# Kernel tuning notes

Measured on AMD Instinct MI355X. Metric: run time of the kernel, lower is better.

## Reference

```python
import jax, jax.numpy as jnp
import numpy as np

RNN = 128
IN = 2
OUT = 2
OBS_LEN = 8
PRED_LEN = 12


def setup_inputs() -> dict:
    key = jax.random.key(0)
    ks = jax.random.split(key, 8)
    B = 32768
    s = 1.0 / np.sqrt(RNN)  # pytorch LSTM/Linear init bound
    u = lambda k, shape: jax.random.uniform(k, shape, jnp.float32, -s, s)
    return {
        "traj_in": jax.random.normal(ks[0], (B, OBS_LEN, IN), jnp.float32),
        "traj_gt": jax.random.normal(ks[1], (B, PRED_LEN, OUT), jnp.float32),
        "W_ih": u(ks[2], (4 * RNN, IN)),
        "W_hh": u(ks[3], (4 * RNN, RNN)),
        "b_ih": u(ks[4], (4 * RNN,)),
        "b_hh": u(ks[5], (4 * RNN,)),
        "W_last": u(ks[6], (OUT, RNN)),
        "b_last": u(ks[7], (OUT,)),
    }


def _lstm_cell(x, h, c, W_ih, W_hh, b_ih, b_hh):
    # PyTorch gate order: i, f, g, o
    gates = x @ W_ih.T + h @ W_hh.T + (b_ih + b_hh)  # [B, 4*RNN]
    i, f, g, o = jnp.split(gates, 4, axis=-1)
    i = jax.nn.sigmoid(i)
    f = jax.nn.sigmoid(f)
    g = jnp.tanh(g)
    o = jax.nn.sigmoid(o)
    c2 = f * c + i * g
    h2 = o * jnp.tanh(c2)
    return h2, c2


def reference(traj_in, traj_gt, W_ih, W_hh, b_ih, b_hh, W_last, b_last):
    B = traj_in.shape[0]
    dt = traj_in.dtype
    h0 = jnp.zeros((B, RNN), dt)
    c0 = jnp.zeros((B, RNN), dt)

    def head(h):
        # relu -> dropout (identity in eval) -> linear
        return jax.nn.relu(h) @ W_last.T + b_last

    def obs_step(carry, x_t):
        h, c = carry
        h, c = _lstm_cell(x_t, h, c, W_ih, W_hh, b_ih, b_hh)
        return (h, c), head(h)

    xs = jnp.swapaxes(traj_in, 0, 1)  # [T, B, 2]
    (h, c), obs_preds = jax.lax.scan(obs_step, (h0, c0), xs)
    traj_t = obs_preds[-1]  # prediction from last observed step

    def pred_step(carry, _):
        t, h, c = carry
        h2, c2 = _lstm_cell(t, h, c, W_ih, W_hh, b_ih, b_hh)
        return (head(h2), h2, c2), t  # emit current pred, then advance

    _, ys = jax.lax.scan(pred_step, (traj_t, h, c), None, length=PRED_LEN)
    traj_pred = jnp.swapaxes(ys, 0, 1)  # [B, pred_len, 2]
    loss = jnp.mean((traj_pred - traj_gt) ** 2)
    return traj_pred, loss
```

## Files before the change

kernel.cpp:

```cpp
#include <hip/hip_runtime.h>

#define OBS 8
#define PREDL 12
#define NCELL 19

#define W_OFF     0
#define H_OFF     98304
#define RH_OFF    131072
#define LDS_BYTES 163840

typedef short short8 __attribute__((ext_vector_type(8)));
typedef float f32x16 __attribute__((ext_vector_type(16)));
struct U128 { unsigned a, b, c, d; };

__device__ __forceinline__ float sigm(float x) {
    return __builtin_amdgcn_rcpf(1.0f + __builtin_amdgcn_exp2f(x * -1.4426950408889634f));
}
__device__ __forceinline__ float tanh_(float x) {
    return __builtin_amdgcn_rcpf(1.0f + __builtin_amdgcn_exp2f(x * -2.8853900817779268f)) * 2.0f - 1.0f;
}
__device__ __forceinline__ unsigned f2bf(float f) {
    unsigned u = __builtin_bit_cast(unsigned, f);
    u += 0x7fffu + ((u >> 16) & 1u);
    return u >> 16;
}
__device__ __forceinline__ unsigned cvtpk(float lo, float hi) {
    unsigned r;
    asm("v_cvt_pk_bf16_f32 %0, %1, %2" : "=v"(r) : "v"(lo), "v"(hi));
    return r;
}

__global__ __attribute__((amdgpu_waves_per_eu(2, 2))) __launch_bounds__(512)
void lstm_persist(const float* __restrict__ traj_in, const float* __restrict__ traj_gt,
                  const float* __restrict__ W_ih, const float* __restrict__ W_hh,
                  const float* __restrict__ b_ih, const float* __restrict__ b_hh,
                  const float* __restrict__ W_last, const float* __restrict__ b_last,
                  float* __restrict__ out, float* __restrict__ wsloss)
{
    extern __shared__ char smem[];
    const int tid  = threadIdx.x;
    const int lane = tid & 63;
    const int wave = tid >> 6;
    const int l31  = lane & 31;
    const int half = lane >> 5;
    const int sw   = (l31 & 15) << 4;
    const int wm   = wave >> 2;
    const int wc   = wave & 3;
    const int col0 = wc * 32;
    const int myrow = wm * 32 + l31;

    for (int it = 0; it < 24; ++it) {
        int i = it * 512 + tid;
        int n = i >> 5, c4 = i & 31;
        const float4 w = *(const float4*)(W_hh + (size_t)n * 128 + c4 * 4);
        uint2 pk = { f2bf(w.x) | (f2bf(w.y) << 16), f2bf(w.z) | (f2bf(w.w) << 16) };
        *(uint2*)(smem + W_OFF + n * 256 + ((c4 * 8) ^ ((n & 15) << 4))) = pk;
    }

    short8 Ee[4];
    #pragma unroll
    for (int gg = 0; gg < 4; ++gg) {
        U128 v = { 0u, 0u, 0u, 0u };
        if (half == 0) {
            int n = gg * 128 + col0 + l31;
            float2 wi = *(const float2*)(W_ih + n * 2);
            float bsum = b_ih[n] + b_hh[n];
            v.a = f2bf(wi.x) | (f2bf(wi.y) << 16);
            v.b = f2bf(bsum);
        }
        Ee[gg] = __builtin_bit_cast(short8, v);
    }
    short8 Bo[8];
    #pragma unroll
    for (int ks = 0; ks < 8; ++ks) {
        const float* p = W_hh + (size_t)(384 + col0 + l31) * 128 + ks * 16 + half * 8;
        float4 u = *(const float4*)p;
        float4 v = *(const float4*)(p + 4);
        U128 q = { f2bf(u.x) | (f2bf(u.y) << 16), f2bf(u.z) | (f2bf(u.w) << 16),
                   f2bf(v.x) | (f2bf(v.y) << 16), f2bf(v.z) | (f2bf(v.w) << 16) };
        Bo[ks] = __builtin_bit_cast(short8, q);
    }
    short8 Wl[8];
    #pragma unroll
    for (int ks = 0; ks < 8; ++ks) {
        U128 q = { 0u, 0u, 0u, 0u };
        if (l31 < 2) {
            const float* p = W_last + l31 * 128 + ks * 16 + half * 8;
            float4 u = *(const float4*)p;
            float4 v = *(const float4*)(p + 4);
            q.a = f2bf(u.x) | (f2bf(u.y) << 16); q.b = f2bf(u.z) | (f2bf(u.w) << 16);
            q.c = f2bf(v.x) | (f2bf(v.y) << 16); q.d = f2bf(v.z) | (f2bf(v.w) << 16);
        }
        Wl[ks] = __builtin_bit_cast(short8, q);
    }
    const float bl0 = b_last[0], bl1 = b_last[1];

    f32x16 zacc{};
    float lossAcc = 0.f;

    for (int g = 0; g < 2; ++g) {
        const int rbase = blockIdx.x * 128 + g * 64;

        for (int i = 0; i < 8; ++i)
            *(unsigned*)(smem + H_OFF + (tid + i * 512) * 4) = 0u;
        __syncthreads();

        float c_[16];
        #pragma unroll
        for (int r = 0; r < 16; ++r) c_[r] = 0.f;

        for (int t = 0; t < NCELL; ++t) {
            const int hcur  = H_OFF  + (t & 1) * 16384;
            const int hnxt  = H_OFF  + ((t & 1) ^ 1) * 16384;
            const int rhcur = RH_OFF + (t & 1) * 16384;
            const int rhnxt = RH_OFF + ((t & 1) ^ 1) * 16384;

            float2 xx = make_float2(0.f, 0.f);
            if (t < OBS) {
                if (half == 0)
                    xx = *(const float2*)(traj_in + ((size_t)(rbase + myrow) * OBS + t) * 2);
            } else {
                short8 rb0 = *(const short8*)(smem + rhcur + myrow * 256 + ((half * 16) ^ sw));
                f32x16 hd = __builtin_amdgcn_mfma_f32_32x32x16_bf16(Wl[0], rb0, zacc, 0, 0, 0);
                #pragma unroll
                for (int ks = 1; ks < 8; ++ks) {
                    short8 rb = *(const short8*)(smem + rhcur + myrow * 256 +
                                                 ((ks * 32 + half * 16) ^ sw));
                    hd = __builtin_amdgcn_mfma_f32_32x32x16_bf16(Wl[ks], rb, hd, 0, 0, 0);
                }
                if (half == 0) {
                    xx.x = hd[0] + bl0;
                    xx.y = hd[1] + bl1;
                    if (wc == 0) {
                        size_t og = ((size_t)(rbase + myrow) * PREDL + (t - OBS)) * 2;
                        float2 gt = *(const float2*)(traj_gt + og);
                        *(float2*)(out + og) = xx;
                        float d0 = xx.x - gt.x, d1 = xx.y - gt.y;
                        lossAcc = fmaf(d0, d0, fmaf(d1, d1, lossAcc));
                    }
                }
            }

            short8 a[8];
            #pragma unroll
            for (int ks = 0; ks < 8; ++ks)
                a[ks] = *(const short8*)(smem + hcur + myrow * 256 + ((ks * 32 + half * 16) ^ sw));

            f32x16 ac0, ac1, ac2, ac3;
            {
                const int bb = (half * 16) ^ sw;
                const char* wb = smem + W_OFF + (col0 + l31) * 256 + bb;
                ac0 = __builtin_amdgcn_mfma_f32_32x32x16_bf16(a[0], *(const short8*)(wb),             zacc, 0, 0, 0);
                ac1 = __builtin_amdgcn_mfma_f32_32x32x16_bf16(a[0], *(const short8*)(wb + 128 * 256), zacc, 0, 0, 0);
                ac2 = __builtin_amdgcn_mfma_f32_32x32x16_bf16(a[0], *(const short8*)(wb + 256 * 256), zacc, 0, 0, 0);
                ac3 = __builtin_amdgcn_mfma_f32_32x32x16_bf16(a[0], Bo[0],                            zacc, 0, 0, 0);
            }
            #pragma unroll
            for (int ks = 1; ks < 8; ++ks) {
                const int bb = (ks * 32 + half * 16) ^ sw;
                const char* wb = smem + W_OFF + (col0 + l31) * 256 + bb;
                short8 bi  = *(const short8*)(wb);
                short8 bf_ = *(const short8*)(wb + 128 * 256);
                short8 bg  = *(const short8*)(wb + 256 * 256);
                ac0 = __builtin_amdgcn_mfma_f32_32x32x16_bf16(a[ks], bi,     ac0, 0, 0, 0);
                ac1 = __builtin_amdgcn_mfma_f32_32x32x16_bf16(a[ks], bf_,    ac1, 0, 0, 0);
                ac2 = __builtin_amdgcn_mfma_f32_32x32x16_bf16(a[ks], bg,     ac2, 0, 0, 0);
                ac3 = __builtin_amdgcn_mfma_f32_32x32x16_bf16(a[ks], Bo[ks], ac3, 0, 0, 0);
            }
            {
                unsigned xv = (half == 0) ? cvtpk(xx.x, xx.y) : 0u;
                U128 ax = { xv, (half == 0) ? 0x00003F80u : 0u, 0u, 0u };
                short8 aext = __builtin_bit_cast(short8, ax);
                ac0 = __builtin_amdgcn_mfma_f32_32x32x16_bf16(aext, Ee[0], ac0, 0, 0, 0);
                ac1 = __builtin_amdgcn_mfma_f32_32x32x16_bf16(aext, Ee[1], ac1, 0, 0, 0);
                ac2 = __builtin_amdgcn_mfma_f32_32x32x16_bf16(aext, Ee[2], ac2, 0, 0, 0);
                ac3 = __builtin_amdgcn_mfma_f32_32x32x16_bf16(aext, Ee[3], ac3, 0, 0, 0);
            }

            const bool doRelu = (t >= OBS - 1);
            #pragma unroll
            for (int r = 0; r < 16; ++r) {
                float iv = sigm(ac0[r]);
                float fv = sigm(ac1[r]);
                float gv = tanh_(ac2[r]);
                float ov = sigm(ac3[r]);
                float cv = fmaf(fv, c_[r], iv * gv);
                c_[r] = cv;
                float hv = ov * tanh_(cv);
                const int row  = (r & 3) + 8 * (r >> 2) + 4 * half;
                const int arow = wm * 32 + row;
                const int baddr = ((col0 + l31) * 2) ^ ((row & 15) << 4);
                float rl = fmaxf(hv, 0.f);
                unsigned hp = cvtpk(hv, rl);
                *(short*)(smem + hnxt + arow * 256 + baddr) = (short)hp;
                if (doRelu)
                    *(short*)(smem + rhnxt + arow * 256 + baddr) = (short)(hp >> 16);
            }
            __syncthreads();
        }

        if (wc == 0) {
            short8 rb0 = *(const short8*)(smem + RH_OFF + 16384 + myrow * 256 + ((half * 16) ^ sw));
            f32x16 hd = __builtin_amdgcn_mfma_f32_32x32x16_bf16(Wl[0], rb0, zacc, 0, 0, 0);
            #pragma unroll
            for (int ks = 1; ks < 8; ++ks) {
                short8 rb = *(const short8*)(smem + RH_OFF + 16384 + myrow * 256 +
                                             ((ks * 32 + half * 16) ^ sw));
                hd = __builtin_amdgcn_mfma_f32_32x32x16_bf16(Wl[ks], rb, hd, 0, 0, 0);
            }
            if (half == 0) {
                float o0 = hd[0] + bl0, o1 = hd[1] + bl1;
                size_t og = ((size_t)(rbase + myrow) * PREDL + (PREDL - 1)) * 2;
                float2 gt = *(const float2*)(traj_gt + og);
                *(float2*)(out + og) = make_float2(o0, o1);
                float d0 = o0 - gt.x, d1 = o1 - gt.y;
                lossAcc = fmaf(d0, d0, fmaf(d1, d1, lossAcc));
            }
        }
        __syncthreads();
    }

    #pragma unroll
    for (int s = 1; s < 64; s <<= 1) lossAcc += __shfl_xor(lossAcc, s, 64);
    float* sred = (float*)(smem + RH_OFF);
    if (lane == 0) sred[wave] = lossAcc;
    __syncthreads();
    if (tid == 0) {
        float s = 0.f;
        #pragma unroll
        for (int i = 0; i < 8; ++i) s += sred[i];
        wsloss[blockIdx.x] = s;
    }
}

__global__ void loss_reduce(const float* __restrict__ wsloss, float* __restrict__ out,
                            int npart, int nelem)
{
    __shared__ float sacc[4];
    int tid = threadIdx.x;
    float v = 0.f;
    for (int j = tid; j < npart; j += 256) v += wsloss[j];
    #pragma unroll
    for (int s = 1; s < 64; s <<= 1) v += __shfl_xor(v, s, 64);
    if ((tid & 63) == 0) sacc[tid >> 6] = v;
    __syncthreads();
    if (tid == 0) out[nelem] = (sacc[0] + sacc[1] + sacc[2] + sacc[3]) / (float)nelem;
}

extern "C" void kernel_launch(void* const* d_in, const int* in_sizes, int n_in,
                              void* d_out, int out_size, void* d_ws, size_t ws_size,
                              hipStream_t stream)
{
    const float* traj_in = (const float*)d_in[0];
    const float* traj_gt = (const float*)d_in[1];
    const float* W_ih    = (const float*)d_in[2];
    const float* W_hh    = (const float*)d_in[3];
    const float* b_ih    = (const float*)d_in[4];
    const float* b_hh    = (const float*)d_in[5];
    const float* W_last  = (const float*)d_in[6];
    const float* b_last  = (const float*)d_in[7];
    float* out = (float*)d_out;
    float* wsloss = (float*)d_ws;

    const int B      = in_sizes[0] / (OBS * 2);
    const int blocks = B / 128;

    lstm_persist<<<blocks, 512, LDS_BYTES, stream>>>(traj_in, traj_gt, W_ih, W_hh,
                                                     b_ih, b_hh, W_last, b_last,
                                                     out, wsloss);
    loss_reduce<<<1, 256, 0, stream>>>(wsloss, out, blocks, out_size - 1);
}
```

Measured before the change: 154.0 us.

## Fold activation scales into weights, interleave gate rows, precompute LDS addresses

Pre-multiplies the gate weights and biases by -log2(e), or -2·log2(e) for the g gate, so the sigmoid and tanh activations skip a multiply per element. It also interleaves the i/f/g weight rows in LDS so each column's three gates sit 256 bytes apart, and hoists all LDS addresses into precomputed per-thread arrays. The intent is to cut VALU work in the elementwise gate loop and address arithmetic in the inner loop. Rounding the pre-scaled weights to bf16 slightly changes numerics, and the address arrays add register pressure.

```diff
diff --git a/kernel.cpp b/kernel.cpp
--- a/kernel.cpp
+++ b/kernel.cpp
@@ -13,11 +13,11 @@
 typedef float f32x16 __attribute__((ext_vector_type(16)));
 struct U128 { unsigned a, b, c, d; };
 
-__device__ __forceinline__ float sigm(float x) {
-    return __builtin_amdgcn_rcpf(1.0f + __builtin_amdgcn_exp2f(x * -1.4426950408889634f));
-}
-__device__ __forceinline__ float tanh_(float x) {
-    return __builtin_amdgcn_rcpf(1.0f + __builtin_amdgcn_exp2f(x * -2.8853900817779268f)) * 2.0f - 1.0f;
+#define NL2E  (-1.4426950408889634f)
+#define N2L2E (-2.8853900817779268f)
+
+__device__ __forceinline__ float sigm_p(float y) {
+    return __builtin_amdgcn_rcpf(1.0f + __builtin_amdgcn_exp2f(y));
 }
 __device__ __forceinline__ unsigned f2bf(float f) {
     unsigned u = __builtin_bit_cast(unsigned, f);
@@ -52,9 +52,12 @@
     for (int it = 0; it < 24; ++it) {
         int i = it * 512 + tid;
         int n = i >> 5, c4 = i & 31;
+        int gi = n >> 7, cn = n & 127;
+        float sc = (gi == 2) ? N2L2E : NL2E;
         const float4 w = *(const float4*)(W_hh + (size_t)n * 128 + c4 * 4);
-        uint2 pk = { f2bf(w.x) | (f2bf(w.y) << 16), f2bf(w.z) | (f2bf(w.w) << 16) };
-        *(uint2*)(smem + W_OFF + n * 256 + ((c4 * 8) ^ ((n & 15) << 4))) = pk;
+        uint2 pk = { f2bf(w.x * sc) | (f2bf(w.y * sc) << 16),
+                     f2bf(w.z * sc) | (f2bf(w.w * sc) << 16) };
+        *(uint2*)(smem + W_OFF + (cn * 3 + gi) * 256 + ((c4 * 8) ^ ((cn & 15) << 4))) = pk;
     }
 
     short8 Ee[4];
@@ -63,9 +66,10 @@
         U128 v = { 0u, 0u, 0u, 0u };
         if (half == 0) {
             int n = gg * 128 + col0 + l31;
+            float sc = (gg == 2) ? N2L2E : NL2E;
             float2 wi = *(const float2*)(W_ih + n * 2);
-            float bsum = b_ih[n] + b_hh[n];
-            v.a = f2bf(wi.x) | (f2bf(wi.y) << 16);
+            float bsum = (b_ih[n] + b_hh[n]) * sc;
+            v.a = f2bf(wi.x * sc) | (f2bf(wi.y * sc) << 16);
             v.b = f2bf(bsum);
         }
         Ee[gg] = __builtin_bit_cast(short8, v);
@@ -76,8 +80,10 @@
         const float* p = W_hh + (size_t)(384 + col0 + l31) * 128 + ks * 16 + half * 8;
         float4 u = *(const float4*)p;
         float4 v = *(const float4*)(p + 4);
-        U128 q = { f2bf(u.x) | (f2bf(u.y) << 16), f2bf(u.z) | (f2bf(u.w) << 16),
-                   f2bf(v.x) | (f2bf(v.y) << 16), f2bf(v.z) | (f2bf(v.w) << 16) };
+        U128 q = { f2bf(u.x * NL2E) | (f2bf(u.y * NL2E) << 16),
+                   f2bf(u.z * NL2E) | (f2bf(u.w * NL2E) << 16),
+                   f2bf(v.x * NL2E) | (f2bf(v.y * NL2E) << 16),
+                   f2bf(v.z * NL2E) | (f2bf(v.w * NL2E) << 16) };
         Bo[ks] = __builtin_bit_cast(short8, q);
     }
     short8 Wl[8];
@@ -95,6 +101,19 @@
     }
     const float bl0 = b_last[0], bl1 = b_last[1];
 
+    int aAddr[8], wAddr[8], hAddr[16];
+    #pragma unroll
+    for (int ks = 0; ks < 8; ++ks) {
+        const int bv = (ks * 32 + half * 16) ^ sw;
+        aAddr[ks] = H_OFF + myrow * 256 + bv;
+        wAddr[ks] = W_OFF + (col0 + l31) * 768 + bv;
+    }
+    #pragma unroll
+    for (int r = 0; r < 16; ++r) {
+        const int row = (r & 3) + 8 * (r >> 2) + 4 * half;
+        hAddr[r] = H_OFF + (wm * 32 + row) * 256 + (((col0 + l31) * 2) ^ ((row & 15) << 4));
+    }
+
     f32x16 zacc{};
     float lossAcc = 0.f;
 
@@ -110,22 +129,19 @@
         for (int r = 0; r < 16; ++r) c_[r] = 0.f;
 
         for (int t = 0; t < NCELL; ++t) {
-            const int hcur  = H_OFF  + (t & 1) * 16384;
-            const int hnxt  = H_OFF  + ((t & 1) ^ 1) * 16384;
-            const int rhcur = RH_OFF + (t & 1) * 16384;
-            const int rhnxt = RH_OFF + ((t & 1) ^ 1) * 16384;
+            const int hparR = (t & 1) * 16384;
+            const int hparW = 16384 - hparR;
 
             float2 xx = make_float2(0.f, 0.f);
             if (t < OBS) {
                 if (half == 0)
                     xx = *(const float2*)(traj_in + ((size_t)(rbase + myrow) * OBS + t) * 2);
             } else {
-                short8 rb0 = *(const short8*)(smem + rhcur + myrow * 256 + ((half * 16) ^ sw));
+                short8 rb0 = *(const short8*)(smem + aAddr[0] + 32768 + hparR);
                 f32x16 hd = __builtin_amdgcn_mfma_f32_32x32x16_bf16(Wl[0], rb0, zacc, 0, 0, 0);
                 #pragma unroll
                 for (int ks = 1; ks < 8; ++ks) {
-                    short8 rb = *(const short8*)(smem + rhcur + myrow * 256 +
-                                                 ((ks * 32 + half * 16) ^ sw));
+                    short8 rb = *(const short8*)(smem + aAddr[ks] + 32768 + hparR);
                     hd = __builtin_amdgcn_mfma_f32_32x32x16_bf16(Wl[ks], rb, hd, 0, 0, 0);
                 }
                 if (half == 0) {
@@ -144,24 +160,22 @@
             short8 a[8];
             #pragma unroll
             for (int ks = 0; ks < 8; ++ks)
-                a[ks] = *(const short8*)(smem + hcur + myrow * 256 + ((ks * 32 + half * 16) ^ sw));
+                a[ks] = *(const short8*)(smem + aAddr[ks] + hparR);
 
             f32x16 ac0, ac1, ac2, ac3;
             {
-                const int bb = (half * 16) ^ sw;
-                const char* wb = smem + W_OFF + (col0 + l31) * 256 + bb;
-                ac0 = __builtin_amdgcn_mfma_f32_32x32x16_bf16(a[0], *(const short8*)(wb),             zacc, 0, 0, 0);
-                ac1 = __builtin_amdgcn_mfma_f32_32x32x16_bf16(a[0], *(const short8*)(wb + 128 * 256), zacc, 0, 0, 0);
-                ac2 = __builtin_amdgcn_mfma_f32_32x32x16_bf16(a[0], *(const short8*)(wb + 256 * 256), zacc, 0, 0, 0);
-                ac3 = __builtin_amdgcn_mfma_f32_32x32x16_bf16(a[0], Bo[0],                            zacc, 0, 0, 0);
+                const char* wb = smem + wAddr[0];
+                ac0 = __builtin_amdgcn_mfma_f32_32x32x16_bf16(a[0], *(const short8*)(wb),       zacc, 0, 0, 0);
+                ac1 = __builtin_amdgcn_mfma_f32_32x32x16_bf16(a[0], *(const short8*)(wb + 256), zacc, 0, 0, 0);
+                ac2 = __builtin_amdgcn_mfma_f32_32x32x16_bf16(a[0], *(const short8*)(wb + 512), zacc, 0, 0, 0);
+                ac3 = __builtin_amdgcn_mfma_f32_32x32x16_bf16(a[0], Bo[0],                      zacc, 0, 0, 0);
             }
             #pragma unroll
             for (int ks = 1; ks < 8; ++ks) {
-                const int bb = (ks * 32 + half * 16) ^ sw;
-                const char* wb = smem + W_OFF + (col0 + l31) * 256 + bb;
+                const char* wb = smem + wAddr[ks];
                 short8 bi  = *(const short8*)(wb);
-                short8 bf_ = *(const short8*)(wb + 128 * 256);
-                short8 bg  = *(const short8*)(wb + 256 * 256);
+                short8 bf_ = *(const short8*)(wb + 256);
+                short8 bg  = *(const short8*)(wb + 512);
                 ac0 = __builtin_amdgcn_mfma_f32_32x32x16_bf16(a[ks], bi,     ac0, 0, 0, 0);
                 ac1 = __builtin_amdgcn_mfma_f32_32x32x16_bf16(a[ks], bf_,    ac1, 0, 0, 0);
                 ac2 = __builtin_amdgcn_mfma_f32_32x32x16_bf16(a[ks], bg,     ac2, 0, 0, 0);
@@ -180,32 +194,29 @@
             const bool doRelu = (t >= OBS - 1);
             #pragma unroll
             for (int r = 0; r < 16; ++r) {
-                float iv = sigm(ac0[r]);
-                float fv = sigm(ac1[r]);
-                float gv = tanh_(ac2[r]);
-                float ov = sigm(ac3[r]);
+                float iv = sigm_p(ac0[r]);
+                float fv = sigm_p(ac1[r]);
+                float gv = fmaf(2.f, sigm_p(ac2[r]), -1.f);
+                float ov = sigm_p(ac3[r]);
                 float cv = fmaf(fv, c_[r], iv * gv);
                 c_[r] = cv;
-                float hv = ov * tanh_(cv);
-                const int row  = (r & 3) + 8 * (r >> 2) + 4 * half;
-                const int arow = wm * 32 + row;
-                const int baddr = ((col0 + l31) * 2) ^ ((row & 15) << 4);
+                float th = fmaf(2.f, sigm_p(cv * N2L2E), -1.f);
+                float hv = ov * th;
                 float rl = fmaxf(hv, 0.f);
                 unsigned hp = cvtpk(hv, rl);
-                *(short*)(smem + hnxt + arow * 256 + baddr) = (short)hp;
+                *(short*)(smem + hAddr[r] + hparW) = (short)hp;
                 if (doRelu)
-                    *(short*)(smem + rhnxt + arow * 256 + baddr) = (short)(hp >> 16);
+                    *(short*)(smem + hAddr[r] + hparW + 32768) = (short)(hp >> 16);
             }
             __syncthreads();
         }
 
         if (wc == 0) {
-            short8 rb0 = *(const short8*)(smem + RH_OFF + 16384 + myrow * 256 + ((half * 16) ^ sw));
+            short8 rb0 = *(const short8*)(smem + aAddr[0] + 49152);
             f32x16 hd = __builtin_amdgcn_mfma_f32_32x32x16_bf16(Wl[0], rb0, zacc, 0, 0, 0);
             #pragma unroll
             for (int ks = 1; ks < 8; ++ks) {
-                short8 rb = *(const short8*)(smem + RH_OFF + 16384 + myrow * 256 +
-                                             ((ks * 32 + half * 16) ^ sw));
+                short8 rb = *(const short8*)(smem + aAddr[ks] + 49152);
                 hd = __builtin_amdgcn_mfma_f32_32x32x16_bf16(Wl[ks], rb, hd, 0, 0, 0);
             }
             if (half == 0) {
```

New measurement: 146.8 us. -4.7%, faster.
